# Performance work log

Measured on AMD Instinct MI355X. Metric: run time of the kernel, lower is better.

Reference implementation:

```python
import jax, jax.numpy as jnp
import numpy as np

B, T, C = 2, 2048, 2048
N_HEAD, N_GROUPS, HEAD_SIZE = 16, 4, 128
Q_PER_KV = N_HEAD // N_GROUPS


def setup_inputs() -> dict:
    key = jax.random.key(0)
    k1, k2, k3 = jax.random.split(key, 3)
    x = jax.random.normal(k1, (B, T, C), dtype=jnp.float32)
    # real RoPE cache: theta_i = 10000^{-2i/d}, cos/sin of shape [T, head_size//2]
    half = HEAD_SIZE // 2
    inv_freq = 1.0 / (10000.0 ** (jnp.arange(0, half, dtype=jnp.float32) / half))
    t = jnp.arange(T, dtype=jnp.float32)
    freqs = t[:, None] * inv_freq[None, :]  # [T, half]
    cos, sin = jnp.cos(freqs), jnp.sin(freqs)
    w_attn = jax.random.normal(k2, (C, (N_HEAD + 2 * N_GROUPS) * HEAD_SIZE), dtype=jnp.float32) * (C ** -0.5)
    w_proj = jax.random.normal(k3, (C, C), dtype=jnp.float32) * (C ** -0.5)
    return {"x": x, "cos": cos, "sin": sin, "w_attn": w_attn, "w_proj": w_proj}


def _apply_rope(x, cos, sin):
    # flash-attn style, interleaved=False: rotate first/second half of rotary dims
    # x: [B, T, H, D], cos/sin: [T, D//2]
    d2 = cos.shape[-1]
    x1, x2 = x[..., :d2], x[..., d2:2 * d2]
    c = cos[None, :, None, :]
    s = sin[None, :, None, :]
    return jnp.concatenate([x1 * c - x2 * s, x1 * s + x2 * c], axis=-1)


def reference(x, cos, sin, w_attn, w_proj):
    Bx, Tx, Cx = x.shape
    qkv = x @ w_attn  # [B, T, (n_head + 2*G)*hs]
    qkv = qkv.reshape(Bx, Tx, N_GROUPS, Q_PER_KV + 2, HEAD_SIZE)
    q = qkv[:, :, :, :Q_PER_KV, :].reshape(Bx, Tx, N_HEAD, HEAD_SIZE)
    k = qkv[:, :, :, Q_PER_KV, :]        # [B, T, G, hs]
    v = qkv[:, :, :, Q_PER_KV + 1, :]    # [B, T, G, hs]
    q = _apply_rope(q, cos, sin)
    k = _apply_rope(k, cos, sin)
    # GQA attention without materializing repeated K/V
    qg = q.reshape(Bx, Tx, N_GROUPS, Q_PER_KV, HEAD_SIZE)
    scale = 1.0 / jnp.sqrt(jnp.float32(HEAD_SIZE))
    scores = jnp.einsum('bqgpd,bkgd->bgpqk', qg, k) * scale  # [B,G,p,T,T]
    attn = jax.nn.softmax(scores, axis=-1)
    y = jnp.einsum('bgpqk,bkgd->bqgpd', attn, v)  # [B,T,G,p,hs]
    y = y.reshape(Bx, Tx, Cx)
    return y @ w_proj
```

## Files before the change

kernel.cpp:

```cpp
#include <hip/hip_runtime.h>
#include <stdint.h>

#define B_ 2
#define T_ 2048
#define C_ 2048
#define NH 16
#define NG 4
#define HS 128

typedef unsigned short u16;
typedef __bf16 bf16_t;
typedef bf16_t bf16x8 __attribute__((ext_vector_type(8)));
typedef float f32x4 __attribute__((ext_vector_type(4)));

__device__ __forceinline__ u16 f2bf(float f) {
    union { float f; uint32_t u; } v; v.f = f;
    uint32_t r = (v.u + 0x7fffu + ((v.u >> 16) & 1u)) >> 16;
    return (u16)r;
}
__device__ __forceinline__ float fast_ex2(float x) {
    float r; asm("v_exp_f32 %0, %1" : "=v"(r) : "v"(x)); return r;
}

__device__ __forceinline__ void transpose_body(const float* __restrict__ W, u16* __restrict__ Wt,
                                               int K, int N, int bx, int by, float (*tile)[33]) {
    int n0 = bx * 32, k0 = by * 32;
    int tx = threadIdx.x & 31, ty = threadIdx.x >> 5;
#pragma unroll
    for (int i = 0; i < 4; i++) {
        int r = ty + i * 8;
        tile[r][tx] = W[(size_t)(k0 + r) * N + (n0 + tx)];
    }
    __syncthreads();
#pragma unroll
    for (int i = 0; i < 4; i++) {
        int r = ty + i * 8;
        Wt[(size_t)(n0 + r) * K + (k0 + tx)] = f2bf(tile[tx][r]);
    }
}

__global__ void k_prep(const float* __restrict__ x, u16* __restrict__ xb,
                       const float* __restrict__ wa, u16* __restrict__ wat,
                       const float* __restrict__ wp, u16* __restrict__ wpt) {
    __shared__ float tile[32][33];
    int bid = blockIdx.x;
    if (bid < 8192) {
        int i = bid * 256 + threadIdx.x;
        float4 f = ((const float4*)x)[i];
        ushort4 o;
        o.x = f2bf(f.x); o.y = f2bf(f.y); o.z = f2bf(f.z); o.w = f2bf(f.w);
        ((ushort4*)xb)[i] = o;
    } else if (bid < 8192 + 6144) {
        int id = bid - 8192;
        transpose_body(wa, wat, 2048, 3072, id % 96, id / 96, tile);
    } else {
        int id = bid - 14336;
        transpose_body(wp, wpt, 2048, 2048, id % 64, id / 64, tile);
    }
}

#define MIDB { __builtin_amdgcn_s_barrier();                              \
               asm volatile("s_waitcnt lgkmcnt(0)" ::: "memory");         \
               __builtin_amdgcn_sched_barrier(0); }
#define ENDB { __builtin_amdgcn_s_barrier(); }
#define VMW4 { asm volatile("s_waitcnt vmcnt(4)" ::: "memory"); }
#define VMW0 { asm volatile("s_waitcnt vmcnt(0)" ::: "memory"); }

__device__ __forceinline__ void stage_half(const u16* __restrict__ g, int r0, int k0,
                                           u16* l, int tid) {
#pragma unroll
    for (int i = 0; i < 2; i++) {
        int c = tid + i * 512;
        int row = c >> 3, sl = c & 7;
        const u16* ga = g + (size_t)(r0 + row) * 2048 + k0 + (sl ^ (row & 7)) * 8;
        __builtin_amdgcn_global_load_lds((const __attribute__((address_space(1))) void*)ga,
                                         (__attribute__((address_space(3))) void*)(l + c * 8),
                                         16, 0, 0);
    }
}

__device__ __forceinline__ void stage_half64(const u16* __restrict__ g, int r0, int k0,
                                             u16* l, int tid) {
    int row = tid >> 3, sl = tid & 7;
    const u16* ga = g + (size_t)(r0 + row) * 2048 + k0 + (sl ^ (row & 7)) * 8;
    __builtin_amdgcn_global_load_lds((const __attribute__((address_space(1))) void*)ga,
                                     (__attribute__((address_space(3))) void*)(l + tid * 8),
                                     16, 0, 0);
}

__device__ __forceinline__ void rd_a(const u16* slot, int mq, int l16, int quad,
                                     bf16x8 (&af)[4][2]) {
#pragma unroll
    for (int mf = 0; mf < 4; mf++) {
        int row = mq * 64 + mf * 16 + l16;
#pragma unroll
        for (int kk = 0; kk < 2; kk++)
            af[mf][kk] = *(const bf16x8*)(slot + row * 64 + ((kk * 4 + quad) ^ (l16 & 7)) * 8);
    }
}

__device__ __forceinline__ void rd_b(const u16* slot, int nq, int sub, int l16, int quad,
                                     bf16x8 (&bs)[2][2]) {
#pragma unroll
    for (int g = 0; g < 2; g++) {
        int row = sub * 64 + (nq * 2 + g) * 16 + l16;
#pragma unroll
        for (int kk = 0; kk < 2; kk++)
            bs[g][kk] = *(const bf16x8*)(slot + row * 64 + ((kk * 4 + quad) ^ (l16 & 7)) * 8);
    }
}

template <int MQ, int NQ>
__device__ __forceinline__ void mm8(f32x4 (&acc)[8][4], const bf16x8 (&af)[4][2],
                                    const bf16x8 (&bs)[2][2]) {
    __builtin_amdgcn_s_setprio(1);
#pragma unroll
    for (int mf = 0; mf < 4; mf++)
#pragma unroll
        for (int g = 0; g < 2; g++)
#pragma unroll
            for (int kk = 0; kk < 2; kk++)
                acc[MQ * 4 + mf][NQ * 2 + g] = __builtin_amdgcn_mfma_f32_16x16x32_bf16(
                    af[mf][kk], bs[g][kk], acc[MQ * 4 + mf][NQ * 2 + g], 0, 0, 0);
    __builtin_amdgcn_s_setprio(0);
}

template <int MQ, int NQ>
__device__ __forceinline__ void mm4(f32x4 (&acc)[4][4], const bf16x8 (&af)[2][2],
                                    const bf16x8 (&bs)[2][2]) {
    __builtin_amdgcn_s_setprio(1);
#pragma unroll
    for (int mf = 0; mf < 2; mf++)
#pragma unroll
        for (int g = 0; g < 2; g++)
#pragma unroll
            for (int kk = 0; kk < 2; kk++)
                acc[MQ * 2 + mf][NQ * 2 + g] = __builtin_amdgcn_mfma_f32_16x16x32_bf16(
                    af[mf][kk], bs[g][kk], acc[MQ * 2 + mf][NQ * 2 + g], 0, 0, 0);
    __builtin_amdgcn_s_setprio(0);
}

__global__ __launch_bounds__(512, 2) void k_gemm_qkv(const u16* __restrict__ A,
                                                     const u16* __restrict__ Bt,
                                                     const float* __restrict__ cosb,
                                                     const float* __restrict__ sinb,
                                                     u16* __restrict__ qa,
                                                     u16* __restrict__ ka,
                                                     u16* __restrict__ vt) {
    extern __shared__ __align__(16) u16 sm[];
    const int tid = threadIdx.x;
    const int wave = tid >> 6, lane = tid & 63;
    const int quad = lane >> 4, l16 = lane & 15;
    const int wr = wave >> 2, wc = wave & 3;
    const int lin = blockIdx.x + 12 * blockIdx.y;
    const int swz = (lin & 7) * 24 + (lin >> 3);
    const int bx = swz % 12, by = swz / 12;
    const int m0 = by * 256;
    const int brow = bx * 256;

    const u16* As0 = sm + (0 * 2 + wr) * 8192;
    const u16* As1 = sm + (1 * 2 + wr) * 8192;
    const u16* Bs0 = sm + 32768 + (0 * 2 + (wc >> 1)) * 8192;
    const u16* Bs1 = sm + 32768 + (1 * 2 + (wc >> 1)) * 8192;

    f32x4 acc[8][4] = {};
    bf16x8 af[4][2], b0[2][2], b1[2][2];

    stage_half(A,  m0,        0,  sm + 0 * 8192, tid);
    stage_half(A,  m0 + 128,  0,  sm + 1 * 8192, tid);
    stage_half(Bt, brow,       0,  sm + 32768 + 0 * 8192, tid);
    stage_half(Bt, brow + 128, 0,  sm + 32768 + 1 * 8192, tid);
    stage_half(Bt, brow,       64, sm + 32768 + 2 * 8192, tid);
    stage_half(Bt, brow + 128, 64, sm + 32768 + 3 * 8192, tid);
    VMW4;
    __builtin_amdgcn_s_barrier();

    for (int i = 0; i < 15; i++) {
        const int k0 = i * 128;
        rd_a(As0, 0, l16, quad, af); rd_b(Bs0, 0, wc & 1, l16, quad, b0);
        stage_half(A, m0, k0 + 64, sm + 2 * 8192, tid);
        MIDB; mm8<0, 0>(acc, af, b0); ENDB;
        rd_b(Bs0, 1, wc & 1, l16, quad, b1);
        stage_half(A, m0 + 128, k0 + 64, sm + 3 * 8192, tid);
        MIDB; mm8<0, 1>(acc, af, b1); ENDB;
        rd_a(As0, 1, l16, quad, af);
        stage_half(Bt, brow, k0 + 128, sm + 32768 + 0 * 8192, tid);
        MIDB; mm8<1, 1>(acc, af, b1); ENDB;
        stage_half(Bt, brow + 128, k0 + 128, sm + 32768 + 1 * 8192, tid);
        MIDB; mm8<1, 0>(acc, af, b0); VMW4; ENDB;
        rd_a(As1, 0, l16, quad, af); rd_b(Bs1, 0, wc & 1, l16, quad, b0);
        stage_half(A, m0, k0 + 128, sm + 0 * 8192, tid);
        MIDB; mm8<0, 0>(acc, af, b0); ENDB;
        rd_b(Bs1, 1, wc & 1, l16, quad, b1);
        stage_half(A, m0 + 128, k0 + 128, sm + 1 * 8192, tid);
        MIDB; mm8<0, 1>(acc, af, b1); ENDB;
        rd_a(As1, 1, l16, quad, af);
        stage_half(Bt, brow, k0 + 192, sm + 32768 + 2 * 8192, tid);
        MIDB; mm8<1, 1>(acc, af, b1); ENDB;
        stage_half(Bt, brow + 128, k0 + 192, sm + 32768 + 3 * 8192, tid);
        MIDB; mm8<1, 0>(acc, af, b0); VMW4; ENDB;
    }
    {
        rd_a(As0, 0, l16, quad, af); rd_b(Bs0, 0, wc & 1, l16, quad, b0);
        stage_half(A, m0, 1984, sm + 2 * 8192, tid);
        MIDB; mm8<0, 0>(acc, af, b0); ENDB;
        rd_b(Bs0, 1, wc & 1, l16, quad, b1);
        stage_half(A, m0 + 128, 1984, sm + 3 * 8192, tid);
        MIDB; mm8<0, 1>(acc, af, b1); ENDB;
        rd_a(As0, 1, l16, quad, af);
        MIDB; mm8<1, 1>(acc, af, b1); ENDB;
        MIDB; mm8<1, 0>(acc, af, b0); VMW0; ENDB;
        rd_a(As1, 0, l16, quad, af); rd_b(Bs1, 0, wc & 1, l16, quad, b0);
        MIDB; mm8<0, 0>(acc, af, b0); ENDB;
        rd_b(Bs1, 1, wc & 1, l16, quad, b1);
        MIDB; mm8<0, 1>(acc, af, b1); ENDB;
        rd_a(As1, 1, l16, quad, af);
        MIDB; mm8<1, 1>(acc, af, b1); ENDB;
        MIDB; mm8<1, 0>(acc, af, b0); ENDB;
    }

    __syncthreads();
    const int s = bx * 2 + (wc >> 1);
    const int stype = s % 6, grp = s / 6;
    const int dhalf = wc & 1;
    const int b = by >> 3;
    const int tb = (by & 7) * 256 + wr * 128;
    const int rid = wr * 2 + (wc >> 1);
    float4* xch = (float4*)sm;

    if (stype < 5 && dhalf == 1) {
#pragma unroll
        for (int mf = 0; mf < 8; mf++)
#pragma unroll
            for (int g = 0; g < 4; g++)
                xch[((rid * 8 + mf) * 4 + g) * 64 + quad * 16 + l16] = *(float4*)&acc[mf][g];
    }
    __syncthreads();
    if (stype < 5) {
        if (dhalf == 0) {
            const float QS = 0.08838834764831845f * 1.44269504088896341f;
            const float sc = (stype < 4) ? QS : 1.0f;
            u16* dst = (stype < 4) ? qa + ((size_t)(b * NH + grp * 4 + stype)) * T_ * 128
                                   : ka + ((size_t)(b * NG + grp)) * T_ * 128;
#pragma unroll
            for (int mf = 0; mf < 8; mf++)
#pragma unroll
                for (int g = 0; g < 4; g++) {
                    float4 x2 = xch[((rid * 8 + mf) * 4 + g) * 64 + quad * 16 + l16];
                    const float* x2p = (const float*)&x2;
                    int d = g * 16 + l16;
#pragma unroll
                    for (int r = 0; r < 4; r++) {
                        int t = tb + mf * 16 + quad * 4 + r;
                        float cc = cosb[t * 64 + d], ss = sinb[t * 64 + d];
                        float x1 = acc[mf][g][r];
                        u16* drow = dst + (size_t)t * 128;
                        drow[d] = f2bf((x1 * cc - x2p[r] * ss) * sc);
                        drow[d + 64] = f2bf((x1 * ss + x2p[r] * cc) * sc);
                    }
                }
        }
    } else {
        size_t vb = ((size_t)(b * NG + grp)) * 128;
#pragma unroll
        for (int mf = 0; mf < 8; mf++)
#pragma unroll
            for (int g = 0; g < 4; g++) {
                int d = dhalf * 64 + g * 16 + l16;
                int t0 = tb + mf * 16 + quad * 4;
                ushort4 o = make_ushort4(f2bf(acc[mf][g][0]), f2bf(acc[mf][g][1]),
                                         f2bf(acc[mf][g][2]), f2bf(acc[mf][g][3]));
                *(ushort4*)(vt + (vb + d) * T_ + t0) = o;
            }
    }
}

__global__ __launch_bounds__(512, 2) void k_gemm_bt(const u16* __restrict__ A,
                                                    const u16* __restrict__ Bt,
                                                    float* __restrict__ C) {
    extern __shared__ __align__(16) u16 sm[];
    const int tid = threadIdx.x;
    const int wave = tid >> 6, lane = tid & 63;
    const int quad = lane >> 4, l16 = lane & 15;
    const int wr = wave >> 2, wc = wave & 3;
    const int bh = wc >> 1, sub = wc & 1;
    const int lin = blockIdx.x + 8 * blockIdx.y;
    const int swz = (lin & 7) * 32 + (lin >> 3);
    const int bx = swz & 7, by = swz >> 3;
    const int m0 = by * 128, n0 = bx * 256;

    const u16* As0 = sm + (0 * 2 + wr) * 4096;
    const u16* As1 = sm + (1 * 2 + wr) * 4096;
    const u16* Bs0 = sm + 16384 + (0 * 2 + bh) * 8192;
    const u16* Bs1 = sm + 16384 + (1 * 2 + bh) * 8192;

    f32x4 acc[4][4] = {};
    bf16x8 af[2][2], b0[2][2], b1[2][2];

    stage_half64(A, m0,       0, sm + 0 * 4096, tid);
    stage_half64(A, m0 + 64,  0, sm + 1 * 4096, tid);
    stage_half(Bt, n0,        0, sm + 16384 + 0 * 8192, tid);
    stage_half(Bt, n0 + 128,  0, sm + 16384 + 1 * 8192, tid);
    stage_half(Bt, n0,       64, sm + 16384 + 2 * 8192, tid);
    stage_half(Bt, n0 + 128, 64, sm + 16384 + 3 * 8192, tid);
    VMW4;
    __builtin_amdgcn_s_barrier();

    for (int i = 0; i < 15; i++) {
        const int k0 = i * 128;
        rd_b(As0, 0, 0, l16, quad, af); rd_b(Bs0, 0, sub, l16, quad, b0);
        stage_half64(A, m0, k0 + 64, sm + 2 * 4096, tid);
        MIDB; mm4<0, 0>(acc, af, b0); ENDB;
        rd_b(Bs0, 1, sub, l16, quad, b1);
        stage_half64(A, m0 + 64, k0 + 64, sm + 3 * 4096, tid);
        MIDB; mm4<0, 1>(acc, af, b1); ENDB;
        rd_b(As0, 1, 0, l16, quad, af);
        stage_half(Bt, n0, k0 + 128, sm + 16384 + 0 * 8192, tid);
        MIDB; mm4<1, 1>(acc, af, b1); ENDB;
        stage_half(Bt, n0 + 128, k0 + 128, sm + 16384 + 1 * 8192, tid);
        MIDB; mm4<1, 0>(acc, af, b0); VMW4; ENDB;
        rd_b(As1, 0, 0, l16, quad, af); rd_b(Bs1, 0, sub, l16, quad, b0);
        stage_half64(A, m0, k0 + 128, sm + 0 * 4096, tid);
        MIDB; mm4<0, 0>(acc, af, b0); ENDB;
        rd_b(Bs1, 1, sub, l16, quad, b1);
        stage_half64(A, m0 + 64, k0 + 128, sm + 1 * 4096, tid);
        MIDB; mm4<0, 1>(acc, af, b1); ENDB;
        rd_b(As1, 1, 0, l16, quad, af);
        stage_half(Bt, n0, k0 + 192, sm + 16384 + 2 * 8192, tid);
        MIDB; mm4<1, 1>(acc, af, b1); ENDB;
        stage_half(Bt, n0 + 128, k0 + 192, sm + 16384 + 3 * 8192, tid);
        MIDB; mm4<1, 0>(acc, af, b0); VMW4; ENDB;
    }
    {
        rd_b(As0, 0, 0, l16, quad, af); rd_b(Bs0, 0, sub, l16, quad, b0);
        stage_half64(A, m0, 1984, sm + 2 * 4096, tid);
        MIDB; mm4<0, 0>(acc, af, b0); ENDB;
        rd_b(Bs0, 1, sub, l16, quad, b1);
        stage_half64(A, m0 + 64, 1984, sm + 3 * 4096, tid);
        MIDB; mm4<0, 1>(acc, af, b1); ENDB;
        rd_b(As0, 1, 0, l16, quad, af);
        MIDB; mm4<1, 1>(acc, af, b1); ENDB;
        MIDB; mm4<1, 0>(acc, af, b0); VMW0; ENDB;
        rd_b(As1, 0, 0, l16, quad, af); rd_b(Bs1, 0, sub, l16, quad, b0);
        MIDB; mm4<0, 0>(acc, af, b0); ENDB;
        rd_b(Bs1, 1, sub, l16, quad, b1);
        MIDB; mm4<0, 1>(acc, af, b1); ENDB;
        rd_b(As1, 1, 0, l16, quad, af);
        MIDB; mm4<1, 1>(acc, af, b1); ENDB;
        MIDB; mm4<1, 0>(acc, af, b0); ENDB;
    }

#pragma unroll
    for (int am = 0; am < 4; am++)
#pragma unroll
        for (int an = 0; an < 4; an++)
#pragma unroll
            for (int r = 0; r < 4; r++) {
                int row = m0 + wr * 64 + am * 16 + quad * 4 + r;
                int col = n0 + wc * 64 + an * 16 + l16;
                C[(size_t)row * C_ + col] = acc[am][an][r];
            }
}

__global__ __launch_bounds__(256, 2) void k_attn(const u16* __restrict__ qa,
                                                 const u16* __restrict__ ka,
                                                 const u16* __restrict__ vt,
                                                 u16* __restrict__ ya) {
    extern __shared__ __align__(16) u16 smem[];
    u16* Ks = smem;
    u16* Vs = smem + 16384;
    const int tid = threadIdx.x;
    const int wave = tid >> 6, lane = tid & 63;
    const int quad = lane >> 4, l16 = lane & 15;
    const int qt = blockIdx.x, h = blockIdx.y, b = blockIdx.z;
    const int g = h >> 2;

    bf16x8 qf[2][4];
    {
        const u16* qbase = qa + (((size_t)(b * NH + h)) * T_ + qt * 128 + wave * 32 + l16) * 128;
#pragma unroll
        for (int t16 = 0; t16 < 2; t16++)
#pragma unroll
            for (int ks = 0; ks < 4; ks++)
                qf[t16][ks] = *(const bf16x8*)(qbase + t16 * 16 * 128 + ks * 32 + quad * 8);
    }
    const u16* kbase = ka + ((size_t)(b * NG + g)) * T_ * 128;
    const u16* vbase = vt + ((size_t)(b * NG + g)) * 128 * T_;

    int kdst[4], ksrc[4], vsrc[4], vdA[4], vdB[4];
#pragma unroll
    for (int i = 0; i < 4; i++) {
        int c = tid + i * 256;
        int row = c >> 4, seg = c & 15;
        kdst[i] = c * 8;
        ksrc[i] = row * 128 + (seg ^ (row & 15)) * 8;
        int d = c >> 3, m = c & 7;
        vsrc[i] = d * T_ + m * 8;
        int segA = (m >> 2) * 4 + (m & 1) * 2;
        int a4 = ((m >> 1) & 1) * 4;
        vdA[i] = d * 64 + (segA ^ (d & 7)) * 8 + a4;
        vdB[i] = d * 64 + ((segA + 1) ^ (d & 7)) * 8 + a4;
    }

    f32x4 yacc[2][8] = {};
    float lsum[2] = {0.f, 0.f};
    uint4 vr[4];
    uint32_t pkA[2][4][2], pkB[2][4][2];
    f32x4 sacc[2][4];

    auto ISSUE_K = [&](int kt) {
        u16* Kn = Ks + (kt & 1) * 8192;
        const u16* kb = kbase + (size_t)kt * 8192;
#pragma unroll
        for (int i = 0; i < 4; i++)
            __builtin_amdgcn_global_load_lds(
                (const __attribute__((address_space(1))) void*)(kb + ksrc[i]),
                (__attribute__((address_space(3))) void*)(Kn + kdst[i]), 16, 0, 0);
    };
    auto LOAD_V = [&](int kt) {
        const u16* vb = vbase + kt * 64;
#pragma unroll
        for (int i = 0; i < 4; i++) vr[i] = *(const uint4*)(vb + vsrc[i]);
    };
    auto WRITE_V = [&](int kt) {
        u16* Vc = Vs + (kt % 3) * 8192;
#pragma unroll
        for (int i = 0; i < 4; i++) {
            *(uint2*)&Vc[vdA[i]] = make_uint2(vr[i].x, vr[i].y);
            *(uint2*)&Vc[vdB[i]] = make_uint2(vr[i].z, vr[i].w);
        }
    };
    auto QK = [&](int kt) {
        const u16* Kc = Ks + (kt & 1) * 8192;
#pragma unroll
        for (int t16 = 0; t16 < 2; t16++)
#pragma unroll
            for (int ni = 0; ni < 4; ni++) sacc[t16][ni] = f32x4{0.f, 0.f, 0.f, 0.f};
        __builtin_amdgcn_s_setprio(1);
#pragma unroll
        for (int ks = 0; ks < 4; ks++) {
#pragma unroll
            for (int ni = 0; ni < 4; ni++) {
                bf16x8 kf = *(const bf16x8*)&Kc[(ni * 16 + l16) * 128 + ((ks * 4 + quad) ^ l16) * 8];
                sacc[0][ni] = __builtin_amdgcn_mfma_f32_16x16x32_bf16(kf, qf[0][ks], sacc[0][ni], 0, 0, 0);
                sacc[1][ni] = __builtin_amdgcn_mfma_f32_16x16x32_bf16(kf, qf[1][ks], sacc[1][ni], 0, 0, 0);
            }
        }
        __builtin_amdgcn_s_setprio(0);
    };
    auto SM = [&](uint32_t (&pk)[2][4][2]) {
#pragma unroll
        for (int t16 = 0; t16 < 2; t16++) {
#pragma unroll
            for (int ni = 0; ni < 4; ni++) {
                float p0 = fast_ex2(sacc[t16][ni][0]);
                float p1 = fast_ex2(sacc[t16][ni][1]);
                float p2 = fast_ex2(sacc[t16][ni][2]);
                float p3 = fast_ex2(sacc[t16][ni][3]);
                lsum[t16] += (p0 + p1) + (p2 + p3);
                asm("v_cvt_pk_bf16_f32 %0, %1, %2" : "=v"(pk[t16][ni][0]) : "v"(p0), "v"(p1));
                asm("v_cvt_pk_bf16_f32 %0, %1, %2" : "=v"(pk[t16][ni][1]) : "v"(p2), "v"(p3));
            }
        }
    };
    auto PV = [&](int kt, uint32_t (&pk)[2][4][2]) {
        const u16* Vc = Vs + (kt % 3) * 8192;
        __builtin_amdgcn_s_setprio(1);
#pragma unroll
        for (int ks2 = 0; ks2 < 2; ks2++) {
            union { uint32_t u[4]; bf16x8 v; } pf0, pf1;
            pf0.u[0] = pk[0][2 * ks2][0];     pf0.u[1] = pk[0][2 * ks2][1];
            pf0.u[2] = pk[0][2 * ks2 + 1][0]; pf0.u[3] = pk[0][2 * ks2 + 1][1];
            pf1.u[0] = pk[1][2 * ks2][0];     pf1.u[1] = pk[1][2 * ks2][1];
            pf1.u[2] = pk[1][2 * ks2 + 1][0]; pf1.u[3] = pk[1][2 * ks2 + 1][1];
#pragma unroll
            for (int tile = 0; tile < 8; tile++) {
                bf16x8 vf = *(const bf16x8*)&Vc[(tile * 16 + l16) * 64 +
                                                ((ks2 * 4 + quad) ^ (l16 & 7)) * 8];
                yacc[0][tile] = __builtin_amdgcn_mfma_f32_16x16x32_bf16(vf, pf0.v, yacc[0][tile], 0, 0, 0);
                yacc[1][tile] = __builtin_amdgcn_mfma_f32_16x16x32_bf16(vf, pf1.v, yacc[1][tile], 0, 0, 0);
            }
        }
        __builtin_amdgcn_s_setprio(0);
    };

    ISSUE_K(0); LOAD_V(0);
    VMW0; WRITE_V(0); __syncthreads();
    ISSUE_K(1); LOAD_V(1);
    QK(0); SM(pkA);
    VMW0; WRITE_V(1); __syncthreads();
    for (int kt = 1; kt <= 29; kt += 2) {
        ISSUE_K(kt + 1); LOAD_V(kt + 1);
        QK(kt); SM(pkB); PV(kt - 1, pkA);
        VMW0; WRITE_V(kt + 1); __syncthreads();
        ISSUE_K(kt + 2); LOAD_V(kt + 2);
        QK(kt + 1); SM(pkA); PV(kt, pkB);
        VMW0; WRITE_V(kt + 2); __syncthreads();
    }
    QK(31); SM(pkB); PV(30, pkA);
    PV(31, pkB);

#pragma unroll
    for (int t16 = 0; t16 < 2; t16++) {
        lsum[t16] += __shfl_xor(lsum[t16], 16);
        lsum[t16] += __shfl_xor(lsum[t16], 32);
    }

    __syncthreads();
#pragma unroll
    for (int t16 = 0; t16 < 2; t16++) {
        float inv = 1.f / lsum[t16];
        int qrow = wave * 32 + t16 * 16 + l16;
#pragma unroll
        for (int tile = 0; tile < 8; tile++) {
#pragma unroll
            for (int cp = 0; cp < 2; cp++) {
                int d = tile * 16 + quad * 4 + cp * 2;
                uint32_t pv = (uint32_t)f2bf(yacc[t16][tile][cp * 2] * inv) |
                              ((uint32_t)f2bf(yacc[t16][tile][cp * 2 + 1] * inv) << 16);
                *(uint32_t*)&smem[qrow * 128 + ((d >> 3) ^ l16) * 8 + (d & 7)] = pv;
            }
        }
    }
    __syncthreads();
#pragma unroll
    for (int i = 0; i < 8; i++) {
        int cc = tid + i * 256;
        int row = cc >> 4, seg = cc & 15;
        uint4 dv = *(const uint4*)&smem[row * 128 + (seg ^ (row & 15)) * 8];
        size_t q = (size_t)(b * T_ + qt * 128 + row);
        *(uint4*)(ya + q * C_ + h * 128 + seg * 8) = dv;
    }
}

extern "C" void kernel_launch(void* const* d_in, const int* in_sizes, int n_in,
                              void* d_out, int out_size, void* d_ws, size_t ws_size,
                              hipStream_t stream) {
    (void)in_sizes; (void)n_in; (void)out_size; (void)ws_size;
    const float* x = (const float*)d_in[0];
    const float* cosb = (const float*)d_in[1];
    const float* sinb = (const float*)d_in[2];
    const float* w_attn = (const float*)d_in[3];
    const float* w_proj = (const float*)d_in[4];
    float* out = (float*)d_out;

    char* ws = (char*)d_ws;
    size_t off = 0;
    auto alloc = [&](size_t bytes) -> char* {
        char* p = ws + off;
        off += (bytes + 255) & ~(size_t)255;
        return p;
    };
    u16* xb  = (u16*)alloc((size_t)4096 * 2048 * 2);
    u16* wat = (u16*)alloc((size_t)3072 * 2048 * 2);
    u16* wpt = (u16*)alloc((size_t)2048 * 2048 * 2);
    u16* qa  = (u16*)alloc((size_t)B_ * NH * T_ * HS * 2);
    u16* ka  = (u16*)alloc((size_t)B_ * NG * T_ * HS * 2);
    u16* vt  = (u16*)alloc((size_t)B_ * NG * T_ * HS * 2);
    u16* ya  = xb;

    static bool smset = false;
    if (!smset) {
        (void)hipFuncSetAttribute((const void*)k_gemm_qkv,
                                  hipFuncAttributeMaxDynamicSharedMemorySize, 131072);
        (void)hipFuncSetAttribute((const void*)k_gemm_bt,
                                  hipFuncAttributeMaxDynamicSharedMemorySize, 98304);
        (void)hipFuncSetAttribute((const void*)k_attn,
                                  hipFuncAttributeMaxDynamicSharedMemorySize, 81920);
        smset = true;
    }

    k_prep<<<dim3(18432), dim3(256), 0, stream>>>(x, xb, w_attn, wat, w_proj, wpt);
    k_gemm_qkv<<<dim3(12, 16), dim3(512), 131072, stream>>>(xb, wat, cosb, sinb, qa, ka, vt);
    k_attn<<<dim3(16, 16, 2), dim3(256), 81920, stream>>>(qa, ka, vt, ya);
    k_gemm_bt<<<dim3(8, 32), dim3(512), 98304, stream>>>(ya, wpt, out);
}
```

Before: 306.6 us.

## Restructure attention loop into single-stage STEP with static double-buffered LDS

Replaces the software-pipelined attention loop, which overlapped QK and softmax of one tile with PV of the previous tile using triple-buffered V, with a simpler per-tile STEP. Each STEP does QK, softmax and PV on the same tile and uses double-buffered K and V in static shared memory. LDS use drops from 80KB dynamic to 64KB static, which may allow more blocks per CU and frees registers from the second softmax buffer. The cost is the loss of the cross-tile overlap between the softmax of one tile and the PV MFMAs of the previous one. Softmax and PV are interleaved in halves, which may recover some of that overlap.

```diff
diff --git a/kernel.cpp b/kernel.cpp
--- a/kernel.cpp
+++ b/kernel.cpp
@@ -366,9 +366,11 @@
                                                  const u16* __restrict__ ka,
                                                  const u16* __restrict__ vt,
                                                  u16* __restrict__ ya) {
-    extern __shared__ __align__(16) u16 smem[];
-    u16* Ks = smem;
-    u16* Vs = smem + 16384;
+    __shared__ __align__(16) u16 smem[32768];
+    u16* const Ks0 = smem;
+    u16* const Ks1 = smem + 8192;
+    u16* const Vs0 = smem + 16384;
+    u16* const Vs1 = smem + 24576;
     const int tid = threadIdx.x;
     const int wave = tid >> 6, lane = tid & 63;
     const int quad = lane >> 4, l16 = lane & 15;
@@ -405,11 +407,8 @@
     f32x4 yacc[2][8] = {};
     float lsum[2] = {0.f, 0.f};
     uint4 vr[4];
-    uint32_t pkA[2][4][2], pkB[2][4][2];
-    f32x4 sacc[2][4];
-
-    auto ISSUE_K = [&](int kt) {
-        u16* Kn = Ks + (kt & 1) * 8192;
+
+    auto ISSUE_K = [&](int kt, u16* Kn) {
         const u16* kb = kbase + (size_t)kt * 8192;
 #pragma unroll
         for (int i = 0; i < 4; i++)
@@ -422,16 +421,18 @@
 #pragma unroll
         for (int i = 0; i < 4; i++) vr[i] = *(const uint4*)(vb + vsrc[i]);
     };
-    auto WRITE_V = [&](int kt) {
-        u16* Vc = Vs + (kt % 3) * 8192;
+    auto WRITE_V = [&](u16* Vc) {
 #pragma unroll
         for (int i = 0; i < 4; i++) {
             *(uint2*)&Vc[vdA[i]] = make_uint2(vr[i].x, vr[i].y);
             *(uint2*)&Vc[vdB[i]] = make_uint2(vr[i].z, vr[i].w);
         }
     };
-    auto QK = [&](int kt) {
-        const u16* Kc = Ks + (kt & 1) * 8192;
+
+    auto STEP = [&](const u16* Kc, const u16* Vc, u16* Kn, u16* Vn, int kt1, bool stage) {
+        if (stage) { ISSUE_K(kt1, Kn); LOAD_V(kt1); }
+
+        f32x4 sacc[2][4];
 #pragma unroll
         for (int t16 = 0; t16 < 2; t16++)
 #pragma unroll
@@ -447,58 +448,58 @@
             }
         }
         __builtin_amdgcn_s_setprio(0);
-    };
-    auto SM = [&](uint32_t (&pk)[2][4][2]) {
-#pragma unroll
-        for (int t16 = 0; t16 < 2; t16++) {
-#pragma unroll
-            for (int ni = 0; ni < 4; ni++) {
-                float p0 = fast_ex2(sacc[t16][ni][0]);
-                float p1 = fast_ex2(sacc[t16][ni][1]);
-                float p2 = fast_ex2(sacc[t16][ni][2]);
-                float p3 = fast_ex2(sacc[t16][ni][3]);
-                lsum[t16] += (p0 + p1) + (p2 + p3);
-                asm("v_cvt_pk_bf16_f32 %0, %1, %2" : "=v"(pk[t16][ni][0]) : "v"(p0), "v"(p1));
-                asm("v_cvt_pk_bf16_f32 %0, %1, %2" : "=v"(pk[t16][ni][1]) : "v"(p2), "v"(p3));
+
+        uint32_t pk[2][4][2];
+#pragma unroll
+        for (int h0 = 0; h0 < 2; h0++) {
+#pragma unroll
+            for (int t16 = 0; t16 < 2; t16++) {
+#pragma unroll
+                for (int nn = 0; nn < 2; nn++) {
+                    const int ni = h0 * 2 + nn;
+                    float p0 = fast_ex2(sacc[t16][ni][0]);
+                    float p1 = fast_ex2(sacc[t16][ni][1]);
+                    float p2 = fast_ex2(sacc[t16][ni][2]);
+                    float p3 = fast_ex2(sacc[t16][ni][3]);
+                    lsum[t16] += (p0 + p1) + (p2 + p3);
+                    asm("v_cvt_pk_bf16_f32 %0, %1, %2" : "=v"(pk[t16][ni][0]) : "v"(p0), "v"(p1));
+                    asm("v_cvt_pk_bf16_f32 %0, %1, %2" : "=v"(pk[t16][ni][1]) : "v"(p2), "v"(p3));
+                }
             }
-        }
-    };
-    auto PV = [&](int kt, uint32_t (&pk)[2][4][2]) {
-        const u16* Vc = Vs + (kt % 3) * 8192;
-        __builtin_amdgcn_s_setprio(1);
-#pragma unroll
-        for (int ks2 = 0; ks2 < 2; ks2++) {
             union { uint32_t u[4]; bf16x8 v; } pf0, pf1;
-            pf0.u[0] = pk[0][2 * ks2][0];     pf0.u[1] = pk[0][2 * ks2][1];
-            pf0.u[2] = pk[0][2 * ks2 + 1][0]; pf0.u[3] = pk[0][2 * ks2 + 1][1];
-            pf1.u[0] = pk[1][2 * ks2][0];     pf1.u[1] = pk[1][2 * ks2][1];
-            pf1.u[2] = pk[1][2 * ks2 + 1][0]; pf1.u[3] = pk[1][2 * ks2 + 1][1];
+            pf0.u[0] = pk[0][2 * h0][0];     pf0.u[1] = pk[0][2 * h0][1];
+            pf0.u[2] = pk[0][2 * h0 + 1][0]; pf0.u[3] = pk[0][2 * h0 + 1][1];
+            pf1.u[0] = pk[1][2 * h0][0];     pf1.u[1] = pk[1][2 * h0][1];
+            pf1.u[2] = pk[1][2 * h0 + 1][0]; pf1.u[3] = pk[1][2 * h0 + 1][1];
+            __builtin_amdgcn_s_setprio(1);
 #pragma unroll
             for (int tile = 0; tile < 8; tile++) {
                 bf16x8 vf = *(const bf16x8*)&Vc[(tile * 16 + l16) * 64 +
-                                                ((ks2 * 4 + quad) ^ (l16 & 7)) * 8];
+                                                ((h0 * 4 + quad) ^ (l16 & 7)) * 8];
                 yacc[0][tile] = __builtin_amdgcn_mfma_f32_16x16x32_bf16(vf, pf0.v, yacc[0][tile], 0, 0, 0);
                 yacc[1][tile] = __builtin_amdgcn_mfma_f32_16x16x32_bf16(vf, pf1.v, yacc[1][tile], 0, 0, 0);
             }
+            __builtin_amdgcn_s_setprio(0);
         }
-        __builtin_amdgcn_s_setprio(0);
+
+        if (stage) {
+            asm volatile("s_waitcnt vmcnt(0)" ::: "memory");
+            WRITE_V(Vn);
+        }
+        __syncthreads();
     };
 
-    ISSUE_K(0); LOAD_V(0);
-    VMW0; WRITE_V(0); __syncthreads();
-    ISSUE_K(1); LOAD_V(1);
-    QK(0); SM(pkA);
-    VMW0; WRITE_V(1); __syncthreads();
-    for (int kt = 1; kt <= 29; kt += 2) {
-        ISSUE_K(kt + 1); LOAD_V(kt + 1);
-        QK(kt); SM(pkB); PV(kt - 1, pkA);
-        VMW0; WRITE_V(kt + 1); __syncthreads();
-        ISSUE_K(kt + 2); LOAD_V(kt + 2);
-        QK(kt + 1); SM(pkA); PV(kt, pkB);
-        VMW0; WRITE_V(kt + 2); __syncthreads();
-    }
-    QK(31); SM(pkB); PV(30, pkA);
-    PV(31, pkB);
+    ISSUE_K(0, Ks0); LOAD_V(0);
+    asm volatile("s_waitcnt vmcnt(0)" ::: "memory");
+    WRITE_V(Vs0);
+    __syncthreads();
+
+    for (int kt = 0; kt < 30; kt += 2) {
+        STEP(Ks0, Vs0, Ks1, Vs1, kt + 1, true);
+        STEP(Ks1, Vs1, Ks0, Vs0, kt + 2, true);
+    }
+    STEP(Ks0, Vs0, Ks1, Vs1, 31, true);
+    STEP(Ks1, Vs1, nullptr, nullptr, 0, false);
 
 #pragma unroll
     for (int t16 = 0; t16 < 2; t16++) {
@@ -506,7 +507,6 @@
         lsum[t16] += __shfl_xor(lsum[t16], 32);
     }
 
-    __syncthreads();
 #pragma unroll
     for (int t16 = 0; t16 < 2; t16++) {
         float inv = 1.f / lsum[t16];
@@ -565,13 +565,11 @@
                                   hipFuncAttributeMaxDynamicSharedMemorySize, 131072);
         (void)hipFuncSetAttribute((const void*)k_gemm_bt,
                                   hipFuncAttributeMaxDynamicSharedMemorySize, 98304);
-        (void)hipFuncSetAttribute((const void*)k_attn,
-                                  hipFuncAttributeMaxDynamicSharedMemorySize, 81920);
         smset = true;
     }
 
     k_prep<<<dim3(18432), dim3(256), 0, stream>>>(x, xb, w_attn, wat, w_proj, wpt);
     k_gemm_qkv<<<dim3(12, 16), dim3(512), 131072, stream>>>(xb, wat, cosb, sinb, qa, ka, vt);
-    k_attn<<<dim3(16, 16, 2), dim3(256), 81920, stream>>>(qa, ka, vt, ya);
+    k_attn<<<dim3(16, 16, 2), dim3(256), 0, stream>>>(qa, ka, vt, ya);
     k_gemm_bt<<<dim3(8, 32), dim3(512), 98304, stream>>>(ya, wpt, out);
 }
```

Measured after the change: 274.7 us. -10.4%, faster.
